# Performance work log

Measured on AMD Instinct MI355X. Metric: run time of the kernel, lower is better.

Reference implementation:

```python
import jax, jax.numpy as jnp
import numpy as np

N = 1 << 19          # active voxels
CIN, COUT = 64, 128
STRIDE = 2
B, T, H, W = 4, 8, 512, 512   # batch_size and spatial_shape [T,H,W]
EPS = 1e-5


def setup_inputs() -> dict:
    key = jax.random.key(0)
    k1, k2, k3, k4, k5, k6 = jax.random.split(key, 6)
    features = jax.random.normal(k1, (N, CIN), dtype=jnp.float32)
    b = jax.random.randint(k2, (N,), 0, B)
    t = jax.random.randint(k3, (N,), 0, T)
    y = jax.random.randint(k4, (N,), 0, H)
    x = jax.random.randint(k5, (N,), 0, W)
    indices = jnp.stack([b, t, y, x], axis=1).astype(jnp.int32)  # [N,4]
    weight = jax.random.normal(k6, (CIN, COUT), dtype=jnp.float32) / np.sqrt(CIN)
    gamma = jnp.ones((COUT,), dtype=jnp.float32)
    beta = jnp.zeros((COUT,), dtype=jnp.float32)
    return {"features": features, "indices": indices, "weight": weight,
            "gamma": gamma, "beta": beta}


def reference(features, indices, weight, gamma, beta):
    # --- sort_sparse_tensor: lexicographic sort via linear index (b,t,y,x) ---
    idx = indices.astype(jnp.int32)
    lin = (idx[:, 0] * (T * H * W) + idx[:, 1] * (H * W)
           + idx[:, 2] * W + idx[:, 3])
    order = jnp.argsort(lin)
    feats = features[order]          # [N, CIN] gathered in sorted order
    sidx = idx[order]                # [N, 4]
    # --- kernel-1 strided sparse conv: only voxels with y%s==0 and x%s==0
    #     survive; per-voxel 1x1 GEMM (bias=False) ---
    mask = (sidx[:, 2] % STRIDE == 0) & (sidx[:, 3] % STRIDE == 0)  # [N]
    out = feats @ weight             # [N, COUT]
    # --- SparseGroupNorm == LayerNorm over channels ---
    mu = jnp.mean(out, axis=-1, keepdims=True)
    var = jnp.mean(jnp.square(out - mu), axis=-1, keepdims=True)
    ln = (out - mu) * jax.lax.rsqrt(var + EPS) * gamma + beta
    # fixed-shape stand-in for spconv's compaction: zero invalid rows,
    # mark their indices -1 (valid rows carry identical math to spconv).
    out_f = jnp.where(mask[:, None], ln, 0.0)
    new_idx = sidx.at[:, 2].set(sidx[:, 2] // STRIDE)
    new_idx = new_idx.at[:, 3].set(new_idx[:, 3] // STRIDE)
    new_idx = jnp.where(mask[:, None], new_idx, -1)
    return out_f, new_idx
```

## Files before the change

### kernel.cpp

```cpp
#include <hip/hip_runtime.h>
#include <stdint.h>

#define N_VOX   (1 << 19)
#define CIN     64
#define COUT    128
#define BIN_SHIFT 3
#define BINS    (1 << 20)
#define OFF_BITS 4
#define BPB     256
#define EPSV    1e-5f

typedef float f32x4 __attribute__((ext_vector_type(4)));
typedef float f32x2 __attribute__((ext_vector_type(2)));

static __device__ __forceinline__ void nt_store4(float* p, f32x4 v) {
    __builtin_nontemporal_store(v, (f32x4*)p);
}
static __device__ __forceinline__ void nt_store2(float* p, f32x2 v) {
    __builtin_nontemporal_store(v, (f32x2*)p);
}


__global__ void k_clear(int* __restrict__ p) {
    int t = blockIdx.x * 256 + threadIdx.x;
    *(int4*)&p[t * 4] = make_int4(0, 0, 0, 0);
}

__global__ void k_hist(const int* __restrict__ idx, unsigned* __restrict__ packed,
                       int* __restrict__ hist) {
    int j = blockIdx.x * 256 + threadIdx.x;
    int4 v = *(const int4*)&idx[j * 4];
    int lin = ((v.x * 8 + v.y) * 512 + v.z) * 512 + v.w;
    int off = atomicAdd(&hist[lin >> BIN_SHIFT], 1);
    packed[j] = ((unsigned)lin << OFF_BITS) | (unsigned)off;
}

__global__ void scan_partial(const int* __restrict__ hist, int* __restrict__ partials) {
    __shared__ int sdata[256];
    int base = blockIdx.x * 1024;
    int t = threadIdx.x;
    int s = hist[base + t] + hist[base + t + 256] + hist[base + t + 512] + hist[base + t + 768];
    sdata[t] = s;
    __syncthreads();
    for (int off = 128; off > 0; off >>= 1) {
        if (t < off) sdata[t] += sdata[t + off];
        __syncthreads();
    }
    if (t == 0) partials[blockIdx.x] = sdata[0];
}

__global__ void scan_top(int* __restrict__ partials) {
    __shared__ int sdata[1024];
    int t = threadIdx.x;
    sdata[t] = partials[t];
    __syncthreads();
    for (int off = 1; off < 1024; off <<= 1) {
        int v = 0;
        if (t >= off) v = sdata[t - off];
        __syncthreads();
        sdata[t] += v;
        __syncthreads();
    }
    partials[t] = t ? sdata[t - 1] : 0;
}

__global__ void scan_final(const int* __restrict__ hist, const int* __restrict__ partials,
                           int* __restrict__ cursor) {
    __shared__ int sscan[256];
    int t = threadIdx.x;
    int base = blockIdx.x * 1024 + t * 4;
    int4 v = *(const int4*)&hist[base];
    int s0 = v.x, s1 = v.x + v.y, s2 = s1 + v.z, s3 = s2 + v.w;
    sscan[t] = s3;
    __syncthreads();
    for (int off = 1; off < 256; off <<= 1) {
        int u = 0;
        if (t >= off) u = sscan[t - off];
        __syncthreads();
        sscan[t] += u;
        __syncthreads();
    }
    int prefix = partials[blockIdx.x] + (t ? sscan[t - 1] : 0);
    int4 e;
    e.x = prefix;
    e.y = prefix + s0;
    e.z = prefix + s1;
    e.w = prefix + s2;
    *(int4*)&cursor[base] = e;
}

__global__ void k_scatter(const unsigned* __restrict__ packed, const int* __restrict__ cursor,
                          int* __restrict__ perm) {
    int j = blockIdx.x * 256 + threadIdx.x;
    unsigned p = packed[j];
    int pos = cursor[p >> (OFF_BITS + BIN_SHIFT)] + (int)(p & ((1u << OFF_BITS) - 1u));
    perm[pos] = j;
}

__global__ __launch_bounds__(256) void k_mega(
    const float* __restrict__ feats, const float* __restrict__ weight,
    const float* __restrict__ gamma, const float* __restrict__ beta,
    const int* __restrict__ hist, const int* __restrict__ cursor,
    const unsigned* __restrict__ packed, int* __restrict__ perm,
    float* __restrict__ out) {
    __shared__ float featb[4][8][CIN];
    __shared__ int wsum[4];
    __shared__ unsigned ibit[32];
    __shared__ unsigned short vpos[384];

    int tid = threadIdx.x;
    int w = tid >> 6, lane = tid & 63;
    int B0 = blockIdx.x * BPB;
    int p0 = cursor[B0];
    int p1 = (B0 + BPB < BINS) ? cursor[B0 + BPB] : N_VOX;
    int npos = p1 - p0;

    if (tid < 32) ibit[tid] = 0;

    int b = B0 + tid;
    int c = hist[b];
    int s = cursor[b];
    if (c >= 2) {
        for (int i = 1; i < c; i++) {
            int pj = perm[s + i];
            unsigned long long kj =
                ((unsigned long long)(packed[pj] >> OFF_BITS) << 19) | (unsigned)pj;
            int m = i - 1;
            while (m >= 0) {
                int pm = perm[s + m];
                unsigned long long km =
                    ((unsigned long long)(packed[pm] >> OFF_BITS) << 19) | (unsigned)pm;
                if (km <= kj) break;
                perm[s + m + 1] = pm;
                m--;
            }
            perm[s + m + 1] = pj;
        }
    }
    int myv = 0;
    for (int i = 0; i < c; i++) {
        unsigned lin = packed[perm[s + i]] >> OFF_BITS;
        myv += ((lin & 0x201u) == 0u) ? 1 : 0;
    }
    int incl = myv;
    #pragma unroll
    for (int off = 1; off < 64; off <<= 1) {
        int u = __shfl_up(incl, off);
        if (lane >= off) incl += u;
    }
    if (lane == 63) wsum[w] = incl;
    __syncthreads();
    int s0 = wsum[0], s1 = wsum[1], s2 = wsum[2], s3 = wsum[3];
    int nv = s0 + s1 + s2 + s3;
    int woff = (w > 0 ? s0 : 0) + (w > 1 ? s1 : 0) + (w > 2 ? s2 : 0);
    int basev = woff + incl - myv;
    for (int i = 0; i < c; i++) {
        int pos = s + i;
        unsigned lin = packed[perm[pos]] >> OFF_BITS;
        int lp = pos - p0;
        if ((lin & 0x201u) == 0u) vpos[basev++] = (unsigned short)lp;
        else atomicOr(&ibit[lp >> 5], 1u << (lp & 31));
    }
    __syncthreads();

    {
        f32x4 mi = {-1.f, -1.f, -1.f, -1.f};
        for (int lp = tid; lp < npos; lp += 256) {
            if ((ibit[lp >> 5] >> (lp & 31)) & 1u)
                nt_store4(&out[(size_t)N_VOX * COUT + (size_t)(p0 + lp) * 4], mi);
        }
        f32x4 z = {0.f, 0.f, 0.f, 0.f};
        for (int lp = w * 2 + (lane >> 5); lp < npos; lp += 8) {
            if ((ibit[lp >> 5] >> (lp & 31)) & 1u)
                nt_store4(&out[(size_t)(p0 + lp) * COUT + (lane & 31) * 4], z);
        }
    }

    if (nv == 0) return;
    const float2* Wg = (const float2*)weight;
    float2 gv = *(const float2*)&gamma[lane * 2];
    float2 bvv = *(const float2*)&beta[lane * 2];

    for (int m0 = 0; m0 < nv; m0 += 32) {
        int mb = m0 + w * 8;
        if (mb >= nv) continue;
        #pragma unroll
        for (int i = 0; i < 8; i++) {
            int m = mb + i;
            int pos = p0 + vpos[(m < nv) ? m : 0];
            featb[w][i][lane] = feats[(size_t)perm[pos] * CIN + lane];
        }

        float2 acc[8];
        #pragma unroll
        for (int i = 0; i < 8; i++) { acc[i].x = 0.f; acc[i].y = 0.f; }

        #pragma unroll 4
        for (int k0 = 0; k0 < CIN; k0 += 4) {
            float2 wv0 = Wg[(k0 + 0) * 64 + lane];
            float2 wv1 = Wg[(k0 + 1) * 64 + lane];
            float2 wv2 = Wg[(k0 + 2) * 64 + lane];
            float2 wv3 = Wg[(k0 + 3) * 64 + lane];
            #pragma unroll
            for (int i = 0; i < 8; i++) {
                float4 f = *(float4*)&featb[w][i][k0];
                acc[i].x = fmaf(f.x, wv0.x, acc[i].x); acc[i].y = fmaf(f.x, wv0.y, acc[i].y);
                acc[i].x = fmaf(f.y, wv1.x, acc[i].x); acc[i].y = fmaf(f.y, wv1.y, acc[i].y);
                acc[i].x = fmaf(f.z, wv2.x, acc[i].x); acc[i].y = fmaf(f.z, wv2.y, acc[i].y);
                acc[i].x = fmaf(f.w, wv3.x, acc[i].x); acc[i].y = fmaf(f.w, wv3.y, acc[i].y);
            }
        }

        #pragma unroll
        for (int i = 0; i < 8; i++) {
            int m = mb + i;
            float v0 = acc[i].x, v1 = acc[i].y;
            float sm = v0 + v1;
            float sq = v0 * v0 + v1 * v1;
            #pragma unroll
            for (int off = 32; off > 0; off >>= 1) {
                sm += __shfl_xor(sm, off);
                sq += __shfl_xor(sq, off);
            }
            float mean = sm * (1.0f / COUT);
            float var  = fmaxf(sq * (1.0f / COUT) - mean * mean, 0.0f);
            float rstd = rsqrtf(var + EPSV);
            if (m < nv) {
                int pos = p0 + vpos[m];
                f32x2 o;
                o.x = (v0 - mean) * rstd * gv.x + bvv.x;
                o.y = (v1 - mean) * rstd * gv.y + bvv.y;
                nt_store2(&out[(size_t)pos * COUT + lane * 2], o);
                if (lane == 0) {
                    unsigned lin = packed[perm[pos]] >> OFF_BITS;
                    f32x4 ni;
                    ni.x = (float)(lin >> 21);
                    ni.y = (float)((lin >> 18) & 7u);
                    ni.z = (float)(((lin >> 9) & 511u) >> 1);
                    ni.w = (float)((lin & 511u) >> 1);
                    nt_store4(&out[(size_t)N_VOX * COUT + (size_t)pos * 4], ni);
                }
            }
        }
    }
}

extern "C" void kernel_launch(void* const* d_in, const int* in_sizes, int n_in,
                              void* d_out, int out_size, void* d_ws, size_t ws_size,
                              hipStream_t stream) {
    const float* feats  = (const float*)d_in[0];
    const int*   idx    = (const int*)d_in[1];
    const float* weight = (const float*)d_in[2];
    const float* gamma  = (const float*)d_in[3];
    const float* beta   = (const float*)d_in[4];
    float* out = (float*)d_out;

    int* ws = (int*)d_ws;
    int*      hist     = ws;
    int*      cursor   = ws + BINS;
    unsigned* packed   = (unsigned*)(ws + 2 * BINS);
    int*      perm     = ws + 2 * BINS + N_VOX;
    int*      partials = ws + 2 * BINS + 2 * N_VOX;

    k_clear<<<BINS / 1024, 256, 0, stream>>>(hist);
    k_hist<<<N_VOX / 256, 256, 0, stream>>>(idx, packed, hist);
    scan_partial<<<BINS / 1024, 256, 0, stream>>>(hist, partials);
    scan_top<<<1, 1024, 0, stream>>>(partials);
    scan_final<<<BINS / 1024, 256, 0, stream>>>(hist, partials, cursor);
    k_scatter<<<N_VOX / 256, 256, 0, stream>>>(packed, cursor, perm);
    k_mega<<<BINS / BPB, 256, 0, stream>>>(feats, weight, gamma, beta,
                                           hist, cursor, packed, perm, out);
}
```

Baseline: 168.3 us.

## Replace three-pass scan with single-pass decoupled lookback and cache sorted keys in LDS

Replaces the three prefix-sum kernels over the bin histogram with one single-pass scan. It takes tile ids from an atomic ticket and uses a decoupled lookback over per-tile status words, which removes two launches and an extra pass over the histogram. The main kernel now keeps each block's permuted indices and linear keys in shared memory instead of re-reading perm and packed from global memory. The GEMM is re-tiled so each half-wave computes four channels per voxel with vector FMAs, which halves the shuffle depth of the LayerNorm reductions. In exchange, the lookback spins serially across tiles, and the fixed shared-memory capacity of 512 voxels per block could overflow on denser inputs.

```diff
diff --git a/kernel.cpp b/kernel.cpp
--- a/kernel.cpp
+++ b/kernel.cpp
@@ -8,22 +8,22 @@
 #define BINS    (1 << 20)
 #define OFF_BITS 4
 #define BPB     256
+#define NTILES  1024
+#define PCAP    512
 #define EPSV    1e-5f
 
 typedef float f32x4 __attribute__((ext_vector_type(4)));
-typedef float f32x2 __attribute__((ext_vector_type(2)));
 
 static __device__ __forceinline__ void nt_store4(float* p, f32x4 v) {
     __builtin_nontemporal_store(v, (f32x4*)p);
 }
-static __device__ __forceinline__ void nt_store2(float* p, f32x2 v) {
-    __builtin_nontemporal_store(v, (f32x2*)p);
-}
-
+
+
+#define CLR_INTS (BINS + 4 + 2 * NTILES)
 
 __global__ void k_clear(int* __restrict__ p) {
     int t = blockIdx.x * 256 + threadIdx.x;
-    *(int4*)&p[t * 4] = make_int4(0, 0, 0, 0);
+    if (t * 4 < CLR_INTS) *(int4*)&p[t * 4] = make_int4(0, 0, 0, 0);
 }
 
 __global__ void k_hist(const int* __restrict__ idx, unsigned* __restrict__ packed,
@@ -35,57 +35,59 @@
     packed[j] = ((unsigned)lin << OFF_BITS) | (unsigned)off;
 }
 
-__global__ void scan_partial(const int* __restrict__ hist, int* __restrict__ partials) {
-    __shared__ int sdata[256];
-    int base = blockIdx.x * 1024;
-    int t = threadIdx.x;
-    int s = hist[base + t] + hist[base + t + 256] + hist[base + t + 512] + hist[base + t + 768];
-    sdata[t] = s;
-    __syncthreads();
-    for (int off = 128; off > 0; off >>= 1) {
-        if (t < off) sdata[t] += sdata[t + off];
-        __syncthreads();
-    }
-    if (t == 0) partials[blockIdx.x] = sdata[0];
-}
-
-__global__ void scan_top(int* __restrict__ partials) {
-    __shared__ int sdata[1024];
-    int t = threadIdx.x;
-    sdata[t] = partials[t];
-    __syncthreads();
-    for (int off = 1; off < 1024; off <<= 1) {
-        int v = 0;
-        if (t >= off) v = sdata[t - off];
-        __syncthreads();
-        sdata[t] += v;
-        __syncthreads();
-    }
-    partials[t] = t ? sdata[t - 1] : 0;
-}
-
-__global__ void scan_final(const int* __restrict__ hist, const int* __restrict__ partials,
-                           int* __restrict__ cursor) {
-    __shared__ int sscan[256];
-    int t = threadIdx.x;
-    int base = blockIdx.x * 1024 + t * 4;
+__global__ __launch_bounds__(256) void k_scan(
+    const int* __restrict__ hist, int* __restrict__ cursor,
+    unsigned long long* __restrict__ tiles, int* __restrict__ ticket) {
+    __shared__ int stile;
+    __shared__ int wsums[4];
+    __shared__ int sprefix;
+    int tid = threadIdx.x;
+    if (tid == 0) stile = atomicAdd(ticket, 1);
+    __syncthreads();
+    int tile = stile;
+    int base = tile * 1024 + tid * 4;
     int4 v = *(const int4*)&hist[base];
-    int s0 = v.x, s1 = v.x + v.y, s2 = s1 + v.z, s3 = s2 + v.w;
-    sscan[t] = s3;
-    __syncthreads();
-    for (int off = 1; off < 256; off <<= 1) {
-        int u = 0;
-        if (t >= off) u = sscan[t - off];
-        __syncthreads();
-        sscan[t] += u;
-        __syncthreads();
-    }
-    int prefix = partials[blockIdx.x] + (t ? sscan[t - 1] : 0);
+    int t3 = v.x + v.y + v.z + v.w;
+    int lane = tid & 63, w = tid >> 6;
+    int incl = t3;
+    #pragma unroll
+    for (int off = 1; off < 64; off <<= 1) {
+        int u = __shfl_up(incl, off);
+        if (lane >= off) incl += u;
+    }
+    if (lane == 63) wsums[w] = incl;
+    __syncthreads();
+    int woff = (w > 0 ? wsums[0] : 0) + (w > 1 ? wsums[1] : 0) + (w > 2 ? wsums[2] : 0);
+    int total = wsums[0] + wsums[1] + wsums[2] + wsums[3];
+    int texcl = woff + incl - t3;
+    if (tid == 0) {
+        unsigned long long st = (tile == 0) ? 2ull : 1ull;
+        unsigned long long val = (tile == 0) ? (unsigned long long)(unsigned)total
+                                             : (unsigned long long)(unsigned)total;
+        atomicExch(&tiles[tile], (st << 40) | val);
+        int pfx = 0;
+        if (tile > 0) {
+            int p = tile - 1;
+            while (true) {
+                unsigned long long d = atomicAdd(&tiles[p], 0ull);
+                unsigned long long st2 = d >> 40;
+                if (st2 == 0) { __builtin_amdgcn_s_sleep(2); continue; }
+                pfx += (int)(unsigned)(d & 0xFFFFFFFFull);
+                if (st2 == 2ull) break;
+                p--;
+            }
+            atomicExch(&tiles[tile],
+                       (2ull << 40) | (unsigned long long)(unsigned)(pfx + total));
+        }
+        sprefix = pfx;
+    }
+    __syncthreads();
+    int prefix = sprefix + texcl;
     int4 e;
     e.x = prefix;
-    e.y = prefix + s0;
-    e.z = prefix + s1;
-    e.w = prefix + s2;
+    e.y = prefix + v.x;
+    e.z = prefix + v.x + v.y;
+    e.w = prefix + v.x + v.y + v.z;
     *(int4*)&cursor[base] = e;
 }
 
@@ -104,9 +106,11 @@
     const unsigned* __restrict__ packed, int* __restrict__ perm,
     float* __restrict__ out) {
     __shared__ float featb[4][8][CIN];
+    __shared__ unsigned slin[PCAP];
+    __shared__ int sperm[PCAP];
+    __shared__ unsigned short vpos[PCAP];
+    __shared__ unsigned ibit[PCAP / 32];
     __shared__ int wsum[4];
-    __shared__ unsigned ibit[32];
-    __shared__ unsigned short vpos[384];
 
     int tid = threadIdx.x;
     int w = tid >> 6, lane = tid & 63;
@@ -115,7 +119,7 @@
     int p1 = (B0 + BPB < BINS) ? cursor[B0 + BPB] : N_VOX;
     int npos = p1 - p0;
 
-    if (tid < 32) ibit[tid] = 0;
+    if (tid < PCAP / 32) ibit[tid] = 0;
 
     int b = B0 + tid;
     int c = hist[b];
@@ -139,7 +143,11 @@
     }
     int myv = 0;
     for (int i = 0; i < c; i++) {
-        unsigned lin = packed[perm[s + i]] >> OFF_BITS;
+        int lp = s - p0 + i;
+        int j = perm[s + i];
+        unsigned lin = packed[j] >> OFF_BITS;
+        slin[lp] = lin;
+        sperm[lp] = j;
         myv += ((lin & 0x201u) == 0u) ? 1 : 0;
     }
     int incl = myv;
@@ -155,13 +163,13 @@
     int woff = (w > 0 ? s0 : 0) + (w > 1 ? s1 : 0) + (w > 2 ? s2 : 0);
     int basev = woff + incl - myv;
     for (int i = 0; i < c; i++) {
-        int pos = s + i;
-        unsigned lin = packed[perm[pos]] >> OFF_BITS;
-        int lp = pos - p0;
-        if ((lin & 0x201u) == 0u) vpos[basev++] = (unsigned short)lp;
+        int lp = s - p0 + i;
+        if ((slin[lp] & 0x201u) == 0u) vpos[basev++] = (unsigned short)lp;
         else atomicOr(&ibit[lp >> 5], 1u << (lp & 31));
     }
     __syncthreads();
+
+    int half = lane >> 5, l32 = lane & 31;
 
     {
         f32x4 mi = {-1.f, -1.f, -1.f, -1.f};
@@ -170,16 +178,16 @@
                 nt_store4(&out[(size_t)N_VOX * COUT + (size_t)(p0 + lp) * 4], mi);
         }
         f32x4 z = {0.f, 0.f, 0.f, 0.f};
-        for (int lp = w * 2 + (lane >> 5); lp < npos; lp += 8) {
+        for (int lp = w * 2 + half; lp < npos; lp += 8) {
             if ((ibit[lp >> 5] >> (lp & 31)) & 1u)
-                nt_store4(&out[(size_t)(p0 + lp) * COUT + (lane & 31) * 4], z);
+                nt_store4(&out[(size_t)(p0 + lp) * COUT + l32 * 4], z);
         }
     }
 
     if (nv == 0) return;
-    const float2* Wg = (const float2*)weight;
-    float2 gv = *(const float2*)&gamma[lane * 2];
-    float2 bvv = *(const float2*)&beta[lane * 2];
+    const f32x4* Wg4 = (const f32x4*)weight;
+    f32x4 gv = *(const f32x4*)&gamma[l32 * 4];
+    f32x4 bv = *(const f32x4*)&beta[l32 * 4];
 
     for (int m0 = 0; m0 < nv; m0 += 32) {
         int mb = m0 + w * 8;
@@ -187,38 +195,38 @@
         #pragma unroll
         for (int i = 0; i < 8; i++) {
             int m = mb + i;
-            int pos = p0 + vpos[(m < nv) ? m : 0];
-            featb[w][i][lane] = feats[(size_t)perm[pos] * CIN + lane];
-        }
-
-        float2 acc[8];
+            int lp = vpos[(m < nv) ? m : 0];
+            featb[w][i][lane] = feats[(size_t)sperm[lp] * CIN + lane];
+        }
+
+        f32x4 acc[4];
         #pragma unroll
-        for (int i = 0; i < 8; i++) { acc[i].x = 0.f; acc[i].y = 0.f; }
+        for (int i = 0; i < 4; i++) acc[i] = (f32x4){0.f, 0.f, 0.f, 0.f};
 
         #pragma unroll 4
         for (int k0 = 0; k0 < CIN; k0 += 4) {
-            float2 wv0 = Wg[(k0 + 0) * 64 + lane];
-            float2 wv1 = Wg[(k0 + 1) * 64 + lane];
-            float2 wv2 = Wg[(k0 + 2) * 64 + lane];
-            float2 wv3 = Wg[(k0 + 3) * 64 + lane];
+            f32x4 wv0 = Wg4[(k0 + 0) * 32 + l32];
+            f32x4 wv1 = Wg4[(k0 + 1) * 32 + l32];
+            f32x4 wv2 = Wg4[(k0 + 2) * 32 + l32];
+            f32x4 wv3 = Wg4[(k0 + 3) * 32 + l32];
             #pragma unroll
-            for (int i = 0; i < 8; i++) {
-                float4 f = *(float4*)&featb[w][i][k0];
-                acc[i].x = fmaf(f.x, wv0.x, acc[i].x); acc[i].y = fmaf(f.x, wv0.y, acc[i].y);
-                acc[i].x = fmaf(f.y, wv1.x, acc[i].x); acc[i].y = fmaf(f.y, wv1.y, acc[i].y);
-                acc[i].x = fmaf(f.z, wv2.x, acc[i].x); acc[i].y = fmaf(f.z, wv2.y, acc[i].y);
-                acc[i].x = fmaf(f.w, wv3.x, acc[i].x); acc[i].y = fmaf(f.w, wv3.y, acc[i].y);
+            for (int ii = 0; ii < 4; ii++) {
+                float4 f = *(float4*)&featb[w][2 * ii + half][k0];
+                acc[ii] += f.x * wv0;
+                acc[ii] += f.y * wv1;
+                acc[ii] += f.z * wv2;
+                acc[ii] += f.w * wv3;
             }
         }
 
         #pragma unroll
-        for (int i = 0; i < 8; i++) {
-            int m = mb + i;
-            float v0 = acc[i].x, v1 = acc[i].y;
-            float sm = v0 + v1;
-            float sq = v0 * v0 + v1 * v1;
+        for (int ii = 0; ii < 4; ii++) {
+            int m = mb + 2 * ii + half;
+            f32x4 a = acc[ii];
+            float sm = a.x + a.y + a.z + a.w;
+            float sq = a.x * a.x + a.y * a.y + a.z * a.z + a.w * a.w;
             #pragma unroll
-            for (int off = 32; off > 0; off >>= 1) {
+            for (int off = 16; off > 0; off >>= 1) {
                 sm += __shfl_xor(sm, off);
                 sq += __shfl_xor(sq, off);
             }
@@ -226,13 +234,12 @@
             float var  = fmaxf(sq * (1.0f / COUT) - mean * mean, 0.0f);
             float rstd = rsqrtf(var + EPSV);
             if (m < nv) {
-                int pos = p0 + vpos[m];
-                f32x2 o;
-                o.x = (v0 - mean) * rstd * gv.x + bvv.x;
-                o.y = (v1 - mean) * rstd * gv.y + bvv.y;
-                nt_store2(&out[(size_t)pos * COUT + lane * 2], o);
-                if (lane == 0) {
-                    unsigned lin = packed[perm[pos]] >> OFF_BITS;
+                int lp = vpos[m];
+                int pos = p0 + lp;
+                f32x4 o = (a - mean) * rstd * gv + bv;
+                nt_store4(&out[(size_t)pos * COUT + l32 * 4], o);
+                if (l32 == 0) {
+                    unsigned lin = slin[lp];
                     f32x4 ni;
                     ni.x = (float)(lin >> 21);
                     ni.y = (float)((lin >> 18) & 7u);
@@ -256,17 +263,16 @@
     float* out = (float*)d_out;
 
     int* ws = (int*)d_ws;
-    int*      hist     = ws;
-    int*      cursor   = ws + BINS;
-    unsigned* packed   = (unsigned*)(ws + 2 * BINS);
-    int*      perm     = ws + 2 * BINS + N_VOX;
-    int*      partials = ws + 2 * BINS + 2 * N_VOX;
-
-    k_clear<<<BINS / 1024, 256, 0, stream>>>(hist);
+    int*                hist   = ws;
+    int*                ticket = ws + BINS;
+    unsigned long long* tiles  = (unsigned long long*)(ws + BINS + 4);
+    int*                cursor = ws + BINS + 4 + 2 * NTILES;
+    unsigned*           packed = (unsigned*)(cursor + BINS);
+    int*                perm   = (int*)(packed + N_VOX);
+
+    k_clear<<<(CLR_INTS / 4 + 255) / 256, 256, 0, stream>>>(ws);
     k_hist<<<N_VOX / 256, 256, 0, stream>>>(idx, packed, hist);
-    scan_partial<<<BINS / 1024, 256, 0, stream>>>(hist, partials);
-    scan_top<<<1, 1024, 0, stream>>>(partials);
-    scan_final<<<BINS / 1024, 256, 0, stream>>>(hist, partials, cursor);
+    k_scan<<<NTILES, 256, 0, stream>>>(hist, cursor, tiles, ticket);
     k_scatter<<<N_VOX / 256, 256, 0, stream>>>(packed, cursor, perm);
     k_mega<<<BINS / BPB, 256, 0, stream>>>(feats, weight, gamma, beta,
                                            hist, cursor, packed, perm, out);
```

Result: no change. 170.6 us (+1.4%).
